# Optimization experiments

Measured on AMD Instinct MI355X. Metric: run time of the kernel, lower is better.

## Reference

```python
import jax, jax.numpy as jnp
import numpy as np
import math

B, N, E, H = 2, 1024, 768, 12
D = E // H  # head_size = 64


def setup_inputs() -> dict:
    key = jax.random.key(0)
    ks = jax.random.split(key, 12)
    node_features = jax.random.normal(ks[0], (B, N, E), dtype=jnp.float32)
    adj = jax.random.bernoulli(ks[1], 0.5, (B, N, N))
    # ensure every row has at least one edge (self-loop) to avoid NaN softmax rows
    adj = adj | jnp.eye(N, dtype=bool)[None]
    key_edge_features = jax.random.normal(ks[2], (B, N, N, D), dtype=jnp.float32)
    s = 1.0 / math.sqrt(E)
    Wq = jax.random.normal(ks[3], (E, E), dtype=jnp.float32) * s
    bq = jnp.zeros((E,), dtype=jnp.float32)
    Wk = jax.random.normal(ks[4], (E, E), dtype=jnp.float32) * s
    bk = jnp.zeros((E,), dtype=jnp.float32)
    Wv = jax.random.normal(ks[5], (E, E), dtype=jnp.float32) * s
    bv = jnp.zeros((E,), dtype=jnp.float32)
    Wo = jax.random.normal(ks[6], (E, E), dtype=jnp.float32) * s
    bo = jnp.zeros((E,), dtype=jnp.float32)
    return dict(node_features=node_features, adj=adj, key_edge_features=key_edge_features,
                Wq=Wq, bq=bq, Wk=Wk, bk=bk, Wv=Wv, bv=bv, Wo=Wo, bo=bo)


def _heads(x):
    # (B, N, E) -> (B, H, N, D)
    return x.reshape(B, N, H, D).transpose(0, 2, 1, 3)


def reference(node_features, adj, key_edge_features, Wq, bq, Wk, bk, Wv, bv, Wo, bo):
    Q = _heads(node_features @ Wq.T + bq)  # (B,H,N,D)
    K = _heads(node_features @ Wk.T + bk)
    V = _heads(node_features @ Wv.T + bv)
    scores = jnp.einsum('bhnd,bhmd->bhnm', Q, K)
    scores = scores + jnp.einsum('bhnd,bnmd->bhnm', Q, key_edge_features)
    scores = scores / jnp.sqrt(jnp.float32(E))  # NOTE: sqrt(embed_dim), faithful to source
    scores = jnp.where(adj[:, None, :, :], scores, -jnp.inf)
    probs = jax.nn.softmax(scores, axis=-1)
    out = jnp.einsum('bhnm,bhmd->bhnd', probs, V)  # (B,H,N,D)
    out = out.transpose(0, 2, 1, 3).reshape(B, N, E)
    return out @ Wo.T + bo
```

## Files before the change

kernel.cpp:

```cpp
#include <hip/hip_runtime.h>
#include <hip/hip_bf16.h>
#include <cstdint>

typedef __attribute__((ext_vector_type(8))) short s16x8;
typedef __attribute__((ext_vector_type(8))) unsigned short u16x8_t;
typedef __attribute__((ext_vector_type(4))) float f32x4_t;
typedef __attribute__((ext_vector_type(4))) unsigned int u32x4_t;
typedef __attribute__((ext_vector_type(4))) unsigned short u16x4_t;

__device__ __forceinline__ unsigned short f2b(float f){
  unsigned u = __float_as_uint(f);
  u += 0x7fffu + ((u>>16)&1u);
  return (unsigned short)(u>>16);
}
__device__ __forceinline__ float b2f(unsigned short s){
  return __uint_as_float(((unsigned)s)<<16);
}
__device__ __forceinline__ unsigned cvt_pk_bf16(float lo, float hi){
  unsigned r;
  asm("v_cvt_pk_bf16_f32 %0, %1, %2" : "=v"(r) : "v"(lo), "v"(hi));
  return r;
}

constexpr float INV_SQRT_E = 0.036084391824351615f;
constexpr float LOG2E = 1.4426950408889634f;

__global__ void k_convert(const float* __restrict__ X,
                          const float* __restrict__ Wq, const float* __restrict__ Wk,
                          const float* __restrict__ Wv, const float* __restrict__ Wo,
                          unsigned short* __restrict__ Xb, unsigned short* __restrict__ Wst){
  const int64_t WTOT = (int64_t)3072*768/4;
  const int64_t XTOT = (int64_t)2048*768/4;
  for (int64_t i = (int64_t)blockIdx.x*blockDim.x + threadIdx.x; i < WTOT+XTOT;
       i += (int64_t)gridDim.x*blockDim.x){
    const float* src; unsigned short* dst;
    if (i < WTOT){
      int64_t e4 = i*4;
      int j = (int)(e4/768), k = (int)(e4 - (int64_t)j*768);
      int w = j/768; int jr = j - w*768;
      const float* Wsel = (w==0)? Wq : (w==1)? Wk : (w==2)? Wv : Wo;
      src = Wsel + (int64_t)jr*768 + k;
      dst = Wst + e4;
    } else {
      int64_t t = (i-WTOT)*4;
      src = X + t; dst = Xb + t;
    }
    f32x4_t v = *reinterpret_cast<const f32x4_t*>(src);
    u16x4_t o;
    o[0]=f2b(v[0]); o[1]=f2b(v[1]); o[2]=f2b(v[2]); o[3]=f2b(v[3]);
    *reinterpret_cast<u16x4_t*>(dst) = o;
  }
}

__launch_bounds__(256)
__global__ void k_gemm(const unsigned short* __restrict__ A,
                       const unsigned short* __restrict__ Wst,
                       const int mode,
                       const float* __restrict__ bq, const float* __restrict__ bk,
                       const float* __restrict__ bv, const float* __restrict__ bo,
                       unsigned short* __restrict__ Qb, unsigned short* __restrict__ Kb,
                       unsigned short* __restrict__ Vt, float* __restrict__ Out){
  __shared__ unsigned short As[64*64];
  __shared__ unsigned short Bs[64*64];
  const int tiles_n = (mode==0)?36:12;
  const int tm = blockIdx.x / tiles_n, tn = blockIdx.x % tiles_n;
  const int row0 = tm*64, col0 = tn*64;
  const unsigned short* Bbase = Wst + (mode==0 ? 0 : (int64_t)2304*768);
  const int tid = threadIdx.x;
  const int lane = tid & 63, wvi = tid >> 6;
  const int l15 = lane & 15, lg = lane >> 4;
  const int wr = (wvi>>1)*32, wc = (wvi&1)*32;
  f32x4_t acc[2][2] = {};
  for (int k0=0;k0<768;k0+=64){
    #pragma unroll
    for (int i=0;i<2;i++){
      int t = tid + i*256;
      int r = t>>3, c8 = t&7;
      u32x4_t va = *reinterpret_cast<const u32x4_t*>(A + (int64_t)(row0+r)*768 + k0 + c8*8);
      u32x4_t vb = *reinterpret_cast<const u32x4_t*>(Bbase + (int64_t)(col0+r)*768 + k0 + c8*8);
      int byt = (t*16) ^ ((r&7)<<4);
      *reinterpret_cast<u32x4_t*>(reinterpret_cast<char*>(As)+byt) = va;
      *reinterpret_cast<u32x4_t*>(reinterpret_cast<char*>(Bs)+byt) = vb;
    }
    __syncthreads();
    #pragma unroll
    for (int ks=0;ks<2;ks++){
      s16x8 af[2], bf[2];
      #pragma unroll
      for (int mt=0;mt<2;mt++){
        int r = wr + mt*16 + l15;
        int byt = (r*128 + ks*64 + lg*16) ^ ((r&7)<<4);
        af[mt] = *reinterpret_cast<const s16x8*>(reinterpret_cast<const char*>(As)+byt);
      }
      #pragma unroll
      for (int nt=0;nt<2;nt++){
        int r = wc + nt*16 + l15;
        int byt = (r*128 + ks*64 + lg*16) ^ ((r&7)<<4);
        bf[nt] = *reinterpret_cast<const s16x8*>(reinterpret_cast<const char*>(Bs)+byt);
      }
      #pragma unroll
      for (int mt=0;mt<2;mt++)
        #pragma unroll
        for (int nt=0;nt<2;nt++)
          acc[mt][nt] = __builtin_amdgcn_mfma_f32_16x16x32_bf16(af[mt], bf[nt], acc[mt][nt], 0,0,0);
    }
    __syncthreads();
  }
  #pragma unroll
  for (int mt=0;mt<2;mt++){
    #pragma unroll
    for (int nt=0;nt<2;nt++){
      int j = col0 + wc + nt*16 + l15;
      #pragma unroll
      for (int r=0;r<4;r++){
        int ii = row0 + wr + mt*16 + lg*4 + r;
        float v = acc[mt][nt][r];
        if (mode==0){
          int w = j/768; int e = j - w*768; int h = e>>6, d = e&63;
          int b = ii>>10, n = ii & 1023;
          if (w==0)      Qb[(((int64_t)(b*12+h)*1024)+n)*64+d] = f2b((v + bq[e])*INV_SQRT_E);
          else if (w==1) Kb[(((int64_t)(b*12+h)*1024)+n)*64+d] = f2b(v + bk[e]);
          else           Vt[(((int64_t)(b*12+h)*64)+d)*1024+n] = f2b(v + bv[e]);
        } else {
          Out[(int64_t)ii*768 + j] = v + bo[j];
        }
      }
    }
  }
}

__launch_bounds__(256,2)
__global__ void k_fused(const unsigned short* __restrict__ Qb, const unsigned short* __restrict__ Kb,
                        const unsigned short* __restrict__ Vt, const int* __restrict__ adj,
                        const float* __restrict__ Ef,
                        float* __restrict__ Onum, float* __restrict__ Lws){
  __shared__ float Sk[12][16][36];
  __shared__ unsigned short Sq[16][12][48];
  __shared__ unsigned short Pb[12][16][32];
  const int bid = blockIdx.x;
  const int mh = bid & 7, qt = (bid>>3) & 63, b = bid >> 9;
  const int q0 = qt*16, mbase = mh*128;
  const int tid = threadIdx.x, lane = tid & 63, wvi = tid>>6;
  const int l15 = lane & 15, lg = lane >> 4;
  const int eq = lane >> 2, mg = lane & 3;

  s16x8 afQ[3][2];
  const unsigned short* vB[3];
  const unsigned short* kB[3];
  #pragma unroll
  for (int hh=0;hh<3;hh++){
    const int h = wvi*3+hh;
    const unsigned short* p = Qb + (((int64_t)(b*12+h)*1024) + q0 + l15)*64;
    afQ[hh][0] = *reinterpret_cast<const s16x8*>(p + lg*8);
    afQ[hh][1] = *reinterpret_cast<const s16x8*>(p + 32 + lg*8);
    vB[hh]  = Vt + ((int64_t)(b*12+h)*64)*1024 + mbase + lg*8;
    kB[hh]  = Kb + ((int64_t)(b*12+h)*1024 + mbase + l15)*64;
  }
  s16x8 bfQ[4][2];
  #pragma unroll
  for (int qq=0;qq<4;qq++){
    s16x8 v0 = {}; s16x8 v1 = {};
    if (l15 < 12){
      const unsigned short* p = Qb + (((int64_t)(b*12+l15)*1024) + q0 + wvi*4 + qq)*64;
      v0 = *reinterpret_cast<const s16x8*>(p + lg*8);
      v1 = *reinterpret_cast<const s16x8*>(p + 32 + lg*8);
    }
    bfQ[qq][0]=v0; bfQ[qq][1]=v1;
  }
  const float* efBase = Ef + (((int64_t)b*1024 + q0 + wvi*4)*1024 + mbase + l15)*64 + lg*8;
  const int*  adjBase = adj + ((int64_t)b*1024 + q0 + wvi*4)*1024 + mbase + lg*4;

  f32x4_t accO[3][4] = {};
  float Lp[3] = {0.f,0.f,0.f};
  f32x4_t eBuf0[8], eBuf1[8];

#define LOAD_E(BUF, QQ, SO) { \
    const float* ep_ = efBase + (int64_t)(QQ)*65536 + (SO)*64; \
    BUF[0] = *reinterpret_cast<const f32x4_t*>(ep_);          \
    BUF[1] = *reinterpret_cast<const f32x4_t*>(ep_+4);        \
    BUF[2] = *reinterpret_cast<const f32x4_t*>(ep_+32);       \
    BUF[3] = *reinterpret_cast<const f32x4_t*>(ep_+36);       \
    BUF[4] = *reinterpret_cast<const f32x4_t*>(ep_+1024);     \
    BUF[5] = *reinterpret_cast<const f32x4_t*>(ep_+1028);     \
    BUF[6] = *reinterpret_cast<const f32x4_t*>(ep_+1056);     \
    BUF[7] = *reinterpret_cast<const f32x4_t*>(ep_+1060);     \
  }
#define QE_COMPUTE(BUF, QQ) { \
    _Pragma("unroll") \
    for (int mt2=0;mt2<2;mt2++){ \
      f32x4_t acc = {0.f,0.f,0.f,0.f}; \
      _Pragma("unroll") \
      for (int ks=0;ks<2;ks++){ \
        f32x4_t lo = BUF[mt2*4+ks*2]; \
        f32x4_t hi = BUF[mt2*4+ks*2+1]; \
        u32x4_t ec; \
        ec[0]=cvt_pk_bf16(lo[0],lo[1]); ec[1]=cvt_pk_bf16(lo[2],lo[3]); \
        ec[2]=cvt_pk_bf16(hi[0],hi[1]); ec[3]=cvt_pk_bf16(hi[2],hi[3]); \
        s16x8 ea = __builtin_bit_cast(s16x8, ec); \
        acc = __builtin_amdgcn_mfma_f32_16x16x32_bf16(ea, bfQ[QQ][ks], acc, 0,0,0); \
      } \
      u32x4_t av = *reinterpret_cast<const u32x4_t*>(adjBase + (QQ)*1024 + so + mt2*16); \
      if (l15 < 12){ \
        u16x4_t o; \
        o[0] = av[0] ? f2b(acc[0]) : (unsigned short)0xFF80; \
        o[1] = av[1] ? f2b(acc[1]) : (unsigned short)0xFF80; \
        o[2] = av[2] ? f2b(acc[2]) : (unsigned short)0xFF80; \
        o[3] = av[3] ? f2b(acc[3]) : (unsigned short)0xFF80; \
        *reinterpret_cast<u16x4_t*>(&Sq[wvi*4+(QQ)][l15][mt2*16 + lg*4]) = o; \
      } \
    } \
  }

  LOAD_E(eBuf0, 0, 0)
  LOAD_E(eBuf1, 1, 0)

  for (int step=0; step<4; step++){
    const int so = step*32;
    if (step) __syncthreads();
    s16x8 vC[3][4];
    #pragma unroll
    for (int hh=0;hh<3;hh++)
      #pragma unroll
      for (int dsb=0;dsb<4;dsb++)
        vC[hh][dsb] = *reinterpret_cast<const s16x8*>(vB[hh] + (int64_t)(dsb*16+l15)*1024 + so);
    #pragma unroll
    for (int hh=0;hh<3;hh++){
      const int h = wvi*3+hh;
      const unsigned short* kp = kB[hh] + so*64;
      #pragma unroll
      for (int mh2=0;mh2<2;mh2++){
        const unsigned short* kr = kp + mh2*16*64;
        f32x4_t a = {0.f,0.f,0.f,0.f};
        s16x8 k0v = *reinterpret_cast<const s16x8*>(kr + lg*8);
        s16x8 k1v = *reinterpret_cast<const s16x8*>(kr + 32 + lg*8);
        a = __builtin_amdgcn_mfma_f32_16x16x32_bf16(afQ[hh][0], k0v, a, 0,0,0);
        a = __builtin_amdgcn_mfma_f32_16x16x32_bf16(afQ[hh][1], k1v, a, 0,0,0);
        #pragma unroll
        for (int r=0;r<4;r++) Sk[h][lg*4+r][mh2*16+l15] = a[r];
      }
    }
    QE_COMPUTE(eBuf0, 0)
    LOAD_E(eBuf0, 2, so)
    QE_COMPUTE(eBuf1, 1)
    LOAD_E(eBuf1, 3, so)
    QE_COMPUTE(eBuf0, 2)
    QE_COMPUTE(eBuf1, 3)
    if (step < 3){
      LOAD_E(eBuf0, 0, so+32)
      LOAD_E(eBuf1, 1, so+32)
    }
    __syncthreads();
    #pragma unroll
    for (int hh=0;hh<3;hh++){
      const int h = wvi*3+hh;
      const float* sr = &Sk[h][eq][mg*8];
      f32x4_t s0 = *reinterpret_cast<const f32x4_t*>(sr);
      f32x4_t s1 = *reinterpret_cast<const f32x4_t*>(sr+4);
      u16x8_t sq = *reinterpret_cast<const u16x8_t*>(&Sq[eq][h][mg*8]);
      float p[8];
      #pragma unroll
      for (int j=0;j<4;j++) p[j]   = exp2f((s0[j] + b2f(sq[j]))*LOG2E);
      #pragma unroll
      for (int j=0;j<4;j++) p[4+j] = exp2f((s1[j] + b2f(sq[4+j]))*LOG2E);
      Lp[hh] += ((p[0]+p[1])+(p[2]+p[3])) + ((p[4]+p[5])+(p[6]+p[7]));
      u32x4_t pk;
      pk[0]=cvt_pk_bf16(p[0],p[1]); pk[1]=cvt_pk_bf16(p[2],p[3]);
      pk[2]=cvt_pk_bf16(p[4],p[5]); pk[3]=cvt_pk_bf16(p[6],p[7]);
      *reinterpret_cast<u32x4_t*>(&Pb[h][eq][mg*8]) = pk;
    }
    #pragma unroll
    for (int hh=0;hh<3;hh++){
      const int h = wvi*3+hh;
      s16x8 pa = *reinterpret_cast<const s16x8*>(&Pb[h][l15][lg*8]);
      #pragma unroll
      for (int dsb=0;dsb<4;dsb++)
        accO[hh][dsb] = __builtin_amdgcn_mfma_f32_16x16x32_bf16(pa, vC[hh][dsb], accO[hh][dsb], 0,0,0);
    }
  }
#undef LOAD_E
#undef QE_COMPUTE
  float* obase = Onum + (int64_t)(b*8+mh)*12*1024*64;
  #pragma unroll
  for (int hh=0;hh<3;hh++){
    const int h = wvi*3+hh;
    #pragma unroll
    for (int dsb=0;dsb<4;dsb++){
      #pragma unroll
      for (int r=0;r<4;r++)
        obase[((int64_t)h*1024 + q0 + lg*4 + r)*64 + dsb*16 + l15] = accO[hh][dsb][r];
    }
  }
  #pragma unroll
  for (int hh=0;hh<3;hh++){
    float Lr = Lp[hh];
    Lr += __shfl_xor(Lr, 1);
    Lr += __shfl_xor(Lr, 2);
    if (mg==0){
      int64_t idx = (((int64_t)(b*8+mh)*12)+(wvi*3+hh))*1024 + q0 + eq;
      Lws[idx] = Lr;
    }
  }
}

__global__ void k_combine(const float* __restrict__ Onum, const float* __restrict__ Lws,
                          unsigned short* __restrict__ A2){
  int64_t t = (int64_t)blockIdx.x*blockDim.x + threadIdx.x;
  if (t >= (int64_t)2*12*1024*64) return;
  const int d = (int)(t & 63);
  const int n = (int)((t>>6) & 1023);
  const int hb = (int)(t>>16);
  const int h = hb % 12, b = hb / 12;
  float num = 0.f, L = 0.f;
  #pragma unroll
  for (int p=0;p<8;p++){
    int64_t base = (((int64_t)(b*8+p)*12)+h)*1024 + n;
    L   += Lws[base];
    num += Onum[base*64 + d];
  }
  A2[((int64_t)(b*1024+n))*768 + h*64 + d] = f2b(num/L);
}

extern "C" void kernel_launch(void* const* d_in, const int* in_sizes, int n_in,
                              void* d_out, int out_size, void* d_ws, size_t ws_size,
                              hipStream_t stream){
  const float* X  = (const float*)d_in[0];
  const int*   adj= (const int*)d_in[1];
  const float* Ef = (const float*)d_in[2];
  const float* Wq = (const float*)d_in[3];
  const float* bq = (const float*)d_in[4];
  const float* Wk = (const float*)d_in[5];
  const float* bk = (const float*)d_in[6];
  const float* Wv = (const float*)d_in[7];
  const float* bv = (const float*)d_in[8];
  const float* Wo = (const float*)d_in[9];
  const float* bo = (const float*)d_in[10];
  char* w = (char*)d_ws;
  unsigned short* Xb = (unsigned short*)(w);
  unsigned short* Wst= (unsigned short*)(w + 3145728);
  unsigned short* Qb = (unsigned short*)(w + 7864320);
  unsigned short* Kb = (unsigned short*)(w + 11010048);
  unsigned short* Vt = (unsigned short*)(w + 14155776);
  float* Onum        = (float*)(w + 67633152);
  float* Lws         = (float*)(w + 117964800);
  unsigned short* A2 = (unsigned short*)(w + 118751232);
  float* Out = (float*)d_out;

  k_convert<<<3840,256,0,stream>>>(X,Wq,Wk,Wv,Wo,Xb,Wst);
  k_gemm<<<1152,256,0,stream>>>(Xb,Wst,0,bq,bk,bv,bo,Qb,Kb,Vt,nullptr);
  k_fused<<<1024,256,0,stream>>>(Qb,Kb,Vt,adj,Ef,Onum,Lws);
  k_combine<<<6144,256,0,stream>>>(Onum,Lws,A2);
  k_gemm<<<384,256,0,stream>>>(A2,Wst,1,bq,bk,bv,bo,nullptr,nullptr,nullptr,Out);
}
```

Measured before the change: 230.7 us.

## Fuse bf16 conversion into GEMM loads and halve attention key split

Removes the separate fp32-to-bf16 conversion kernel by converting X and weight tiles inside the GEMM load loop. Also halves the number of key-range partitions in the fused attention kernel (4 instead of 8, with each block processing 256 keys), which halves the partial numerator/denominator workspace written and reduced by the combine kernel. This trades fewer, longer attention blocks (less parallelism and overlap) and redundant per-tile weight conversion for less workspace traffic and one fewer launch.

```diff
diff --git a/kernel.cpp b/kernel.cpp
--- a/kernel.cpp
+++ b/kernel.cpp
@@ -25,36 +25,10 @@
 constexpr float INV_SQRT_E = 0.036084391824351615f;
 constexpr float LOG2E = 1.4426950408889634f;
 
-__global__ void k_convert(const float* __restrict__ X,
-                          const float* __restrict__ Wq, const float* __restrict__ Wk,
-                          const float* __restrict__ Wv, const float* __restrict__ Wo,
-                          unsigned short* __restrict__ Xb, unsigned short* __restrict__ Wst){
-  const int64_t WTOT = (int64_t)3072*768/4;
-  const int64_t XTOT = (int64_t)2048*768/4;
-  for (int64_t i = (int64_t)blockIdx.x*blockDim.x + threadIdx.x; i < WTOT+XTOT;
-       i += (int64_t)gridDim.x*blockDim.x){
-    const float* src; unsigned short* dst;
-    if (i < WTOT){
-      int64_t e4 = i*4;
-      int j = (int)(e4/768), k = (int)(e4 - (int64_t)j*768);
-      int w = j/768; int jr = j - w*768;
-      const float* Wsel = (w==0)? Wq : (w==1)? Wk : (w==2)? Wv : Wo;
-      src = Wsel + (int64_t)jr*768 + k;
-      dst = Wst + e4;
-    } else {
-      int64_t t = (i-WTOT)*4;
-      src = X + t; dst = Xb + t;
-    }
-    f32x4_t v = *reinterpret_cast<const f32x4_t*>(src);
-    u16x4_t o;
-    o[0]=f2b(v[0]); o[1]=f2b(v[1]); o[2]=f2b(v[2]); o[3]=f2b(v[3]);
-    *reinterpret_cast<u16x4_t*>(dst) = o;
-  }
-}
-
 __launch_bounds__(256)
-__global__ void k_gemm(const unsigned short* __restrict__ A,
-                       const unsigned short* __restrict__ Wst,
+__global__ void k_gemm(const float* __restrict__ X, const unsigned short* __restrict__ A2,
+                       const float* __restrict__ Wq, const float* __restrict__ Wk,
+                       const float* __restrict__ Wv, const float* __restrict__ Wo,
                        const int mode,
                        const float* __restrict__ bq, const float* __restrict__ bk,
                        const float* __restrict__ bv, const float* __restrict__ bo,
@@ -65,7 +39,9 @@
   const int tiles_n = (mode==0)?36:12;
   const int tm = blockIdx.x / tiles_n, tn = blockIdx.x % tiles_n;
   const int row0 = tm*64, col0 = tn*64;
-  const unsigned short* Bbase = Wst + (mode==0 ? 0 : (int64_t)2304*768);
+  const int wsel = (mode==0) ? (col0/768) : 3;
+  const float* Wsel = (wsel==0)? Wq : (wsel==1)? Wk : (wsel==2)? Wv : Wo;
+  const int jr0 = (mode==0) ? (col0 - wsel*768) : col0;
   const int tid = threadIdx.x;
   const int lane = tid & 63, wvi = tid >> 6;
   const int l15 = lane & 15, lg = lane >> 4;
@@ -76,8 +52,23 @@
     for (int i=0;i<2;i++){
       int t = tid + i*256;
       int r = t>>3, c8 = t&7;
-      u32x4_t va = *reinterpret_cast<const u32x4_t*>(A + (int64_t)(row0+r)*768 + k0 + c8*8);
-      u32x4_t vb = *reinterpret_cast<const u32x4_t*>(Bbase + (int64_t)(col0+r)*768 + k0 + c8*8);
+      u32x4_t va, vb;
+      if (mode==0){
+        const float* as = X + (int64_t)(row0+r)*768 + k0 + c8*8;
+        f32x4_t a0 = *reinterpret_cast<const f32x4_t*>(as);
+        f32x4_t a1 = *reinterpret_cast<const f32x4_t*>(as+4);
+        va[0]=cvt_pk_bf16(a0[0],a0[1]); va[1]=cvt_pk_bf16(a0[2],a0[3]);
+        va[2]=cvt_pk_bf16(a1[0],a1[1]); va[3]=cvt_pk_bf16(a1[2],a1[3]);
+      } else {
+        va = *reinterpret_cast<const u32x4_t*>(A2 + (int64_t)(row0+r)*768 + k0 + c8*8);
+      }
+      {
+        const float* bs = Wsel + (int64_t)(jr0+r)*768 + k0 + c8*8;
+        f32x4_t b0 = *reinterpret_cast<const f32x4_t*>(bs);
+        f32x4_t b1 = *reinterpret_cast<const f32x4_t*>(bs+4);
+        vb[0]=cvt_pk_bf16(b0[0],b0[1]); vb[1]=cvt_pk_bf16(b0[2],b0[3]);
+        vb[2]=cvt_pk_bf16(b1[0],b1[1]); vb[3]=cvt_pk_bf16(b1[2],b1[3]);
+      }
       int byt = (t*16) ^ ((r&7)<<4);
       *reinterpret_cast<u32x4_t*>(reinterpret_cast<char*>(As)+byt) = va;
       *reinterpret_cast<u32x4_t*>(reinterpret_cast<char*>(Bs)+byt) = vb;
@@ -138,8 +129,8 @@
   __shared__ unsigned short Sq[16][12][48];
   __shared__ unsigned short Pb[12][16][32];
   const int bid = blockIdx.x;
-  const int mh = bid & 7, qt = (bid>>3) & 63, b = bid >> 9;
-  const int q0 = qt*16, mbase = mh*128;
+  const int mh = bid & 3, qt = (bid>>2) & 63, b = bid >> 8;
+  const int q0 = qt*16, mbase = mh*256;
   const int tid = threadIdx.x, lane = tid & 63, wvi = tid>>6;
   const int l15 = lane & 15, lg = lane >> 4;
   const int eq = lane >> 2, mg = lane & 3;
@@ -214,7 +205,7 @@
   LOAD_E(eBuf0, 0, 0)
   LOAD_E(eBuf1, 1, 0)
 
-  for (int step=0; step<4; step++){
+  for (int step=0; step<8; step++){
     const int so = step*32;
     if (step) __syncthreads();
     s16x8 vC[3][4];
@@ -245,7 +236,7 @@
     LOAD_E(eBuf1, 3, so)
     QE_COMPUTE(eBuf0, 2)
     QE_COMPUTE(eBuf1, 3)
-    if (step < 3){
+    if (step < 7){
       LOAD_E(eBuf0, 0, so+32)
       LOAD_E(eBuf1, 1, so+32)
     }
@@ -279,7 +270,7 @@
   }
 #undef LOAD_E
 #undef QE_COMPUTE
-  float* obase = Onum + (int64_t)(b*8+mh)*12*1024*64;
+  float* obase = Onum + (int64_t)(b*4+mh)*12*1024*64;
   #pragma unroll
   for (int hh=0;hh<3;hh++){
     const int h = wvi*3+hh;
@@ -296,7 +287,7 @@
     Lr += __shfl_xor(Lr, 1);
     Lr += __shfl_xor(Lr, 2);
     if (mg==0){
-      int64_t idx = (((int64_t)(b*8+mh)*12)+(wvi*3+hh))*1024 + q0 + eq;
+      int64_t idx = (((int64_t)(b*4+mh)*12)+(wvi*3+hh))*1024 + q0 + eq;
       Lws[idx] = Lr;
     }
   }
@@ -312,8 +303,8 @@
   const int h = hb % 12, b = hb / 12;
   float num = 0.f, L = 0.f;
   #pragma unroll
-  for (int p=0;p<8;p++){
-    int64_t base = (((int64_t)(b*8+p)*12)+h)*1024 + n;
+  for (int p=0;p<4;p++){
+    int64_t base = (((int64_t)(b*4+p)*12)+h)*1024 + n;
     L   += Lws[base];
     num += Onum[base*64 + d];
   }
@@ -335,8 +326,6 @@
   const float* Wo = (const float*)d_in[9];
   const float* bo = (const float*)d_in[10];
   char* w = (char*)d_ws;
-  unsigned short* Xb = (unsigned short*)(w);
-  unsigned short* Wst= (unsigned short*)(w + 3145728);
   unsigned short* Qb = (unsigned short*)(w + 7864320);
   unsigned short* Kb = (unsigned short*)(w + 11010048);
   unsigned short* Vt = (unsigned short*)(w + 14155776);
@@ -345,9 +334,8 @@
   unsigned short* A2 = (unsigned short*)(w + 118751232);
   float* Out = (float*)d_out;
 
-  k_convert<<<3840,256,0,stream>>>(X,Wq,Wk,Wv,Wo,Xb,Wst);
-  k_gemm<<<1152,256,0,stream>>>(Xb,Wst,0,bq,bk,bv,bo,Qb,Kb,Vt,nullptr);
-  k_fused<<<1024,256,0,stream>>>(Qb,Kb,Vt,adj,Ef,Onum,Lws);
+  k_gemm<<<1152,256,0,stream>>>(X,nullptr,Wq,Wk,Wv,Wo,0,bq,bk,bv,bo,Qb,Kb,Vt,nullptr);
+  k_fused<<<512,256,0,stream>>>(Qb,Kb,Vt,adj,Ef,Onum,Lws);
   k_combine<<<6144,256,0,stream>>>(Onum,Lws,A2);
-  k_gemm<<<384,256,0,stream>>>(A2,Wst,1,bq,bk,bv,bo,nullptr,nullptr,nullptr,Out);
-}
+  k_gemm<<<384,256,0,stream>>>(nullptr,A2,Wq,Wk,Wv,Wo,1,bq,bk,bv,bo,nullptr,nullptr,nullptr,Out);
+}
```

After: 233.3 us. Within noise of the previous version (+1.1%).
